# Kernel tuning notes

Hardware: AMD Instinct MI355X
Metric: run time of the kernel (lower is better)

## Reference

```python
import jax, jax.numpy as jnp
import numpy as np

EPS = 0.1
P, C, T_MLP, C_MLP, B = 196, 768, 384, 3072, 64


def yat(x, W, b, alpha):
    # x: (..., in), W: (out, in), b: (out,), alpha: (1,)
    dot_nb = jnp.einsum('...i,oi->...o', x, W)          # no-bias dot (shared GEMM)
    dot = dot_nb + b
    w_norm_sq = jnp.sum(W * W, axis=1)                   # (out,)
    x_norm_sq = jnp.sum(x * x, axis=-1, keepdims=True)   # (..., 1)
    dist_sq = w_norm_sq + x_norm_sq - 2.0 * dot_nb
    out_f = W.shape[0]
    scale_base = out_f / np.log(out_f + 1.0)
    scale = jnp.sqrt(jnp.asarray(scale_base, x.dtype)) ** alpha[0]
    return scale * (dot * dot) / (dist_sq + EPS)


def setup_inputs() -> dict:
    key = jax.random.key(0)
    ks = jax.random.split(key, 7)
    x = jax.random.normal(ks[0], (B, P, C), dtype=jnp.float32)
    # token-mixing YAT: in=P, out=T_MLP
    tw = jax.random.normal(ks[1], (T_MLP, P), dtype=jnp.float32) / np.sqrt(P)
    tb = jnp.zeros((T_MLP,), jnp.float32)
    t_alpha = jnp.ones((1,), jnp.float32)
    # token-mixing linear: T_MLP -> P
    w2 = jax.random.uniform(ks[2], (P, T_MLP), jnp.float32, -1, 1) / np.sqrt(T_MLP)
    b2 = jax.random.uniform(ks[3], (P,), jnp.float32, -1, 1) / np.sqrt(T_MLP)
    # channel-mixing YAT: in=C, out=C_MLP
    cw = jax.random.normal(ks[4], (C_MLP, C), dtype=jnp.float32) / np.sqrt(C)
    cb = jnp.zeros((C_MLP,), jnp.float32)
    c_alpha = jnp.ones((1,), jnp.float32)
    # channel-mixing linear: C_MLP -> C
    w4 = jax.random.uniform(ks[5], (C, C_MLP), jnp.float32, -1, 1) / np.sqrt(C_MLP)
    b4 = jax.random.uniform(ks[6], (C,), jnp.float32, -1, 1) / np.sqrt(C_MLP)
    return {"x": x, "tw": tw, "tb": tb, "t_alpha": t_alpha, "w2": w2, "b2": b2,
            "cw": cw, "cb": cb, "c_alpha": c_alpha, "w4": w4, "b4": b4}


def reference(x, tw, tb, t_alpha, w2, b2, cw, cb, c_alpha, w4, b4):
    # Token mixing (operates over patch dim)
    shortcut = x
    xt = jnp.swapaxes(x, 1, 2)                 # (B, C, P)
    h = yat(xt, tw, tb, t_alpha)               # (B, C, T_MLP)
    h = jnp.einsum('bct,pt->bcp', h, w2) + b2  # (B, C, P)
    x = shortcut + jnp.swapaxes(h, 1, 2)
    # Channel mixing (operates over hidden dim)
    shortcut = x
    h = yat(x, cw, cb, c_alpha)                # (B, P, C_MLP)
    h = jnp.einsum('bpm,cm->bpc', h, w4) + b4  # (B, P, C)
    return shortcut + h
```

## Files before the change

### kernel.cpp

```cpp
#include <hip/hip_runtime.h>
#include <hip/hip_bf16.h>
#include <math.h>

#define B_   64
#define P_   196
#define PPAD 224
#define C_   768
#define TM_  384
#define CM_  3072
#define EPSY 0.1f

typedef unsigned short u16;
typedef __attribute__((ext_vector_type(8))) short bf16x8;
typedef __attribute__((ext_vector_type(4))) float f32x4;

__device__ __forceinline__ float bf2f(u16 v) {
    return __uint_as_float(((unsigned int)v) << 16);
}
__device__ __forceinline__ u16 f2bf(float f) {
    unsigned int u = __float_as_uint(f);
    unsigned int rounding = 0x7FFFu + ((u >> 16) & 1u);
    return (u16)((u + rounding) >> 16);
}

__device__ __forceinline__ void gl_lds16(const u16* g, u16* l) {
    __builtin_amdgcn_global_load_lds(
        (const __attribute__((address_space(1))) unsigned int*)g,
        (__attribute__((address_space(3))) unsigned int*)l,
        16, 0, 0);
}


__global__ __launch_bounds__(256) void k_prep_xT(const float* __restrict__ x,
                                                 u16* __restrict__ xT,
                                                 float* __restrict__ xn1) {
    __shared__ u16 tile[32][33];
    __shared__ float colsum[32];
    const int b = blockIdx.z, p0 = blockIdx.x * 32, c0 = blockIdx.y * 32;
    const int tx = threadIdx.x & 31, ty = threadIdx.x >> 5;
    if (threadIdx.x < 32) colsum[threadIdx.x] = 0.f;
    const float* xb = x + (size_t)b * P_ * C_;
    float s = 0.f;
    #pragma unroll
    for (int r = 0; r < 4; ++r) {
        int p = p0 + ty + r * 8;
        float v = (p < P_) ? xb[(size_t)p * C_ + c0 + tx] : 0.f;
        u16 h = f2bf(v);
        tile[ty + r * 8][tx] = h;
        float vb = bf2f(h);
        s = fmaf(vb, vb, s);
    }
    __syncthreads();
    u16* dst = xT + ((size_t)b * C_ + c0) * PPAD + p0;
    #pragma unroll
    for (int r = 0; r < 4; ++r) {
        int cl = ty + r * 8;
        dst[(size_t)cl * PPAD + tx] = tile[tx][cl];
    }
    atomicAdd(&colsum[tx], s);
    __syncthreads();
    if (threadIdx.x < 32)
        atomicAdd(&xn1[(size_t)b * C_ + c0 + threadIdx.x], colsum[threadIdx.x]);
}

__device__ __forceinline__ void pad_norm_body(const float* in, u16* outb, float* norm,
                                              int rows, int inlen, int outlen,
                                              int bid, int tid) {
    int wave = (bid * 256 + tid) >> 6;
    int lane = tid & 63;
    if (wave >= rows) return;
    const float* src = in + (size_t)wave * inlen;
    u16* dst = outb + (size_t)wave * outlen;
    float s = 0.f;
    for (int i = lane; i < outlen; i += 64) {
        float v = (i < inlen) ? src[i] : 0.f;
        u16 h = f2bf(v);
        dst[i] = h;
        float vv = bf2f(h);
        s = fmaf(vv, vv, s);
    }
    #pragma unroll
    for (int off = 32; off > 0; off >>= 1) s += __shfl_down(s, off, 64);
    if (lane == 0) norm[wave] = s;
}

__global__ __launch_bounds__(256) void k_prep_weights(
    const float* __restrict__ tw, u16* __restrict__ twb, float* __restrict__ twn,
    const float* __restrict__ cw, u16* __restrict__ cwb, float* __restrict__ cwn,
    const float* __restrict__ w2, u16* __restrict__ w2b,
    const float* __restrict__ w4, u16* __restrict__ w4b) {
    int bid = blockIdx.x, tid = threadIdx.x;
    if (bid < 96) {
        pad_norm_body(tw, twb, twn, TM_, P_, PPAD, bid, tid);
    } else if (bid < 864) {
        pad_norm_body(cw, cwb, cwn, CM_, C_, C_, bid - 96, tid);
    } else if (bid < 1248) {
        int idx = (bid - 864) * 256 + tid;
        int row = idx / TM_;
        w2b[idx] = (row < P_) ? f2bf(w2[(size_t)row * TM_ + (idx % TM_)]) : (u16)0;
    } else {
        int idx = (bid - 1248) * 256 + tid;
        float4 v = ((const float4*)w4)[idx];
        ushort4 o;
        o.x = f2bf(v.x); o.y = f2bf(v.y); o.z = f2bf(v.z); o.w = f2bf(v.w);
        ((ushort4*)w4b)[idx] = o;
    }
}

__device__ __forceinline__ void mfma_mainloop(
    const u16* __restrict__ A, const u16* __restrict__ B,
    int lda, int ldb, int kiters,
    f32x4 (&acc)[4][4], u16* As, u16* Bs) {
    const int t = threadIdx.x;
    const int w = t >> 6, l = t & 63;
    const int quad = l >> 4, l15 = l & 15;
    const int row0 = t >> 2, kc = (t & 3) * 8;

    const u16* pa0 = A + (size_t)row0 * lda + kc;
    const u16* pa1 = A + (size_t)(64 + row0) * lda + kc;
    const u16* pb0 = B + (size_t)row0 * ldb + kc;
    const u16* pb1 = B + (size_t)(64 + row0) * ldb + kc;

    u16* ldsA0 = As + w * 512;
    u16* ldsA1 = As + 2048 + w * 512;
    u16* ldsB0 = Bs + w * 512;
    u16* ldsB1 = Bs + 2048 + w * 512;

#define STAGE_(bsel, koff)                          \
    do {                                            \
        const int nb_ = (bsel) * 4096;              \
        gl_lds16(pa0 + (koff), ldsA0 + nb_);        \
        gl_lds16(pa1 + (koff), ldsA1 + nb_);        \
        gl_lds16(pb0 + (koff), ldsB0 + nb_);        \
        gl_lds16(pb1 + (koff), ldsB1 + nb_);        \
    } while (0)

    STAGE_(0, 0);
    if (kiters > 1) {
        STAGE_(1, 32);
        asm volatile("s_waitcnt vmcnt(4)" ::: "memory");
    } else {
        asm volatile("s_waitcnt vmcnt(0)" ::: "memory");
    }
    __builtin_amdgcn_s_barrier();

    int cur = 0;
    int koff = 64;
    for (int it = 0; it < kiters; ++it) {
        const u16* Aw = As + cur * 4096 + (w >> 1) * 2048;
        const u16* Bw = Bs + cur * 4096 + (w & 1) * 2048;
        bf16x8 af[4], bfr[4];
        #pragma unroll
        for (int i = 0; i < 4; ++i)
            af[i] = *(const bf16x8*)(Aw + ((i * 16 + l15) * 32 + quad * 8));
        #pragma unroll
        for (int j = 0; j < 4; ++j)
            bfr[j] = *(const bf16x8*)(Bw + ((j * 16 + l15) * 32 + quad * 8));
        asm volatile("s_waitcnt lgkmcnt(0)" ::: "memory");
        __builtin_amdgcn_sched_barrier(0);
        __builtin_amdgcn_s_barrier();
        const bool more2 = (it + 2 < kiters);
        if (more2) { STAGE_(cur, koff); koff += 32; }
        __builtin_amdgcn_s_setprio(1);
        #pragma unroll
        for (int i = 0; i < 4; ++i)
            #pragma unroll
            for (int j = 0; j < 4; ++j)
                acc[i][j] = __builtin_amdgcn_mfma_f32_16x16x32_bf16(af[i], bfr[j], acc[i][j], 0, 0, 0);
        __builtin_amdgcn_s_setprio(0);
        if (it + 1 < kiters) {
            if (more2) asm volatile("s_waitcnt vmcnt(4)" ::: "memory");
            else       asm volatile("s_waitcnt vmcnt(0)" ::: "memory");
            __builtin_amdgcn_s_barrier();
        }
        cur ^= 1;
    }
#undef STAGE_
}

#define MFMA_CORE(AP, BP, LDA, LDB, KITERS)                              \
    __shared__ u16 As[2 * 128 * 32];                                     \
    __shared__ u16 Bs[2 * 128 * 32];                                     \
    const int t = threadIdx.x;                                           \
    const int wid = t >> 6, lane = t & 63;                               \
    const int quad = lane >> 4, l15 = lane & 15;                         \
    f32x4 acc[4][4];                                                     \
    _Pragma("unroll")                                                    \
    for (int i = 0; i < 4; ++i)                                          \
        _Pragma("unroll")                                                \
        for (int j = 0; j < 4; ++j) acc[i][j] = (f32x4){0.f,0.f,0.f,0.f};\
    mfma_mainloop(AP, BP, LDA, LDB, KITERS, acc, As, Bs);                \
    const int rbase = m0 + (wid >> 1) * 64;                              \
    const int cbase = n0 + (wid & 1) * 64;

#define PH_MID()  do { __builtin_amdgcn_sched_barrier(0);                 \
    __builtin_amdgcn_s_barrier();                                         \
    asm volatile("s_waitcnt lgkmcnt(0)" ::: "memory");                    \
    __builtin_amdgcn_sched_barrier(0);                                    \
    __builtin_amdgcn_s_setprio(1); } while (0)
#define PH_END()  do { __builtin_amdgcn_s_setprio(0);                     \
    __builtin_amdgcn_sched_barrier(0);                                    \
    __builtin_amdgcn_s_barrier(); } while (0)
#define PH_END_VM(n) do { __builtin_amdgcn_s_setprio(0);                  \
    asm volatile("s_waitcnt vmcnt(" #n ")" ::: "memory");                 \
    __builtin_amdgcn_sched_barrier(0);                                    \
    __builtin_amdgcn_s_barrier(); } while (0)

#define STG16(isB, d, h, T)                                               \
    gl_lds16(((isB) ? gB : gA) + (size_t)((h) * 128 + srow) *             \
                 ((isB) ? ldb : lda) + (T) * 64 + scol,                   \
             smem + ((isB) ? 32768 : 0) + (d) * 16384 + (h) * 8192 + t * 8)

#define DSA16(d, mh, Ar)                                                  \
    _Pragma("unroll")                                                     \
    for (int mi = 0; mi < 2; ++mi) {                                      \
        Ar[mi][0] = *(const bf16x8*)(aB0 + (d) * 16384 + ((mh) * 2 + mi) * 1024); \
        Ar[mi][1] = *(const bf16x8*)(aB1 + (d) * 16384 + ((mh) * 2 + mi) * 1024); \
    }
#define DSB16(d, nh, Br)                                                  \
    _Pragma("unroll")                                                     \
    for (int ni = 0; ni < 2; ++ni) {                                      \
        Br[ni][0] = *(const bf16x8*)(bB0 + (d) * 16384 + ((nh) * 2 + ni) * 1024); \
        Br[ni][1] = *(const bf16x8*)(bB1 + (d) * 16384 + ((nh) * 2 + ni) * 1024); \
    }
#define MMQ16(mh, nh, Br)                                                 \
    _Pragma("unroll")                                                     \
    for (int kk = 0; kk < 2; ++kk)                                        \
        _Pragma("unroll")                                                 \
        for (int mi = 0; mi < 2; ++mi)                                    \
            _Pragma("unroll")                                             \
            for (int ni = 0; ni < 2; ++ni)                                \
                acc[(mh) * 2 + mi][(nh) * 2 + ni] =                       \
                    __builtin_amdgcn_mfma_f32_16x16x32_bf16(              \
                        a[mi][kk], Br[ni][kk],                            \
                        acc[(mh) * 2 + mi][(nh) * 2 + ni], 0, 0, 0);

__device__ __forceinline__ void mfma16w_mainloop(
    const u16* __restrict__ A, const u16* __restrict__ B,
    int lda, int ldb, int ntiles,
    f32x4 (&acc)[4][4], u16* smem) {
    const int t = threadIdx.x;
    const int w = t >> 6, lane = t & 63;
    const int wr = w >> 2, wc = w & 3;
    const int quad = lane >> 4, l15 = lane & 15;

    const int srow = t >> 3;
    const int scol = (((t & 7) ^ (srow & 7)) << 3);
    const u16* gA = A;
    const u16* gB = B;

    const int q = (quad * 8) ^ ((l15 & 7) << 3);
    const u16* aB0 = smem + (wr * 64 + l15) * 64 + q;
    const u16* aB1 = smem + (wr * 64 + l15) * 64 + (q ^ 32);
    const u16* bB0 = smem + 32768 + (wc * 64 + l15) * 64 + q;
    const u16* bB1 = smem + 32768 + (wc * 64 + l15) * 64 + (q ^ 32);

    STG16(1, 0, 0, 0); STG16(1, 0, 1, 0);
    STG16(0, 0, 0, 0); STG16(0, 0, 1, 0);
    STG16(1, 1, 0, 1); STG16(1, 1, 1, 1);
    asm volatile("s_waitcnt vmcnt(2)" ::: "memory");
    __builtin_amdgcn_s_barrier();

    bf16x8 a[2][2], b[2][2], c[2][2];
    const int NI = ntiles >> 1;
    for (int i = 0; i < NI - 1; ++i) {
        const int T1 = 2 * i + 1, N0 = 2 * i + 2, N1 = 2 * i + 3;
        DSA16(0, 0, a) DSB16(0, 0, b)
        STG16(0, 1, 0, T1);
        PH_MID(); MMQ16(0, 0, b) PH_END();
        DSB16(0, 1, c)
        STG16(0, 1, 1, T1);
        PH_MID(); MMQ16(0, 1, c) PH_END();
        DSA16(0, 1, a)
        STG16(1, 0, 0, N0);
        PH_MID(); MMQ16(1, 1, c) PH_END();
        STG16(1, 0, 1, N0);
        PH_MID(); MMQ16(1, 0, b) PH_END_VM(2);
        DSA16(1, 0, a) DSB16(1, 0, b)
        STG16(0, 0, 0, N0);
        PH_MID(); MMQ16(0, 0, b) PH_END();
        DSB16(1, 1, c)
        STG16(0, 0, 1, N0);
        PH_MID(); MMQ16(0, 1, c) PH_END();
        DSA16(1, 1, a)
        STG16(1, 1, 0, N1);
        PH_MID(); MMQ16(1, 1, c) PH_END();
        STG16(1, 1, 1, N1);
        PH_MID(); MMQ16(1, 0, b) PH_END_VM(2);
    }
    {
        const int T1 = ntiles - 1;
        DSA16(0, 0, a) DSB16(0, 0, b)
        STG16(0, 1, 0, T1);
        PH_MID(); MMQ16(0, 0, b) PH_END();
        DSB16(0, 1, c)
        STG16(0, 1, 1, T1);
        PH_MID(); MMQ16(0, 1, c) PH_END();
        DSA16(0, 1, a)
        PH_MID(); MMQ16(1, 1, c) PH_END();
        PH_MID(); MMQ16(1, 0, b) PH_END_VM(0);
        DSA16(1, 0, a) DSB16(1, 0, b)
        PH_MID(); MMQ16(0, 0, b) PH_END();
        DSB16(1, 1, c)
        PH_MID(); MMQ16(0, 1, c) PH_END();
        DSA16(1, 1, a)
        PH_MID(); MMQ16(1, 1, c) PH_END();
        PH_MID(); MMQ16(1, 0, b)
        __builtin_amdgcn_s_setprio(0);
    }
}

__global__ __launch_bounds__(256) void k1_token_yat(
    const u16* __restrict__ xT, const u16* __restrict__ twb,
    const float* __restrict__ tb, const float* __restrict__ twn,
    const float* __restrict__ xn1, const float* __restrict__ alpha, float sb,
    u16* __restrict__ h1) {
    const int m0 = (blockIdx.x + blockIdx.y * 8) * 128;
    const int n0 = blockIdx.z * 128;
    MFMA_CORE(xT + (size_t)m0 * PPAD, twb + (size_t)n0 * PPAD, PPAD, PPAD, PPAD / 32)
    float scale = powf(sqrtf(sb), alpha[0]);
    #pragma unroll
    for (int i = 0; i < 4; ++i) {
        #pragma unroll
        for (int j = 0; j < 4; ++j) {
            int col = cbase + j * 16 + l15;
            float bn = tb[col], wnn = twn[col];
            #pragma unroll
            for (int reg = 0; reg < 4; ++reg) {
                int row = rbase + i * 16 + quad * 4 + reg;
                float dnb = acc[i][j][reg];
                float dot = dnb + bn;
                float dist = wnn + xn1[row] - 2.f * dnb;
                h1[(size_t)row * TM_ + col] = f2bf(scale * dot * dot / (dist + EPSY));
            }
        }
    }
}

__global__ __launch_bounds__(1024) void k3_chan_yat(
    const u16* __restrict__ x1b, const u16* __restrict__ cwb,
    const float* __restrict__ cb, const float* __restrict__ cwn,
    const float* __restrict__ xn2, const float* __restrict__ alpha, float sb,
    u16* __restrict__ h3) {
    __shared__ __align__(16) u16 smem[65536];
    const int mt = blockIdx.x + blockIdx.y * 8;
    if (mt >= (B_ * P_) / 256) return;
    const int m0 = mt * 256;
    const int n0 = blockIdx.z * 256;
    const int t = threadIdx.x;
    const int w = t >> 6, l = t & 63;
    const int wr = w >> 2, wc = w & 3;
    const int quad = l >> 4, l15 = l & 15;
    f32x4 acc[4][4];
    #pragma unroll
    for (int m = 0; m < 4; ++m)
        #pragma unroll
        for (int n = 0; n < 4; ++n) acc[m][n] = (f32x4){0.f, 0.f, 0.f, 0.f};
    mfma16w_mainloop(x1b + (size_t)m0 * C_, cwb + (size_t)n0 * C_,
                     C_, C_, C_ / 64, acc, smem);
    const int rbase = m0 + wr * 64;
    const int cbase = n0 + wc * 64;
    float scale = powf(sqrtf(sb), alpha[0]);
    #pragma unroll
    for (int m = 0; m < 4; ++m) {
        #pragma unroll
        for (int n = 0; n < 4; ++n) {
            int col = cbase + n * 16 + l15;
            float bn = cb[col], wnn = cwn[col];
            #pragma unroll
            for (int reg = 0; reg < 4; ++reg) {
                int row = rbase + m * 16 + quad * 4 + reg;
                float dnb = acc[m][n][reg];
                float dot = dnb + bn;
                float dist = wnn + xn2[row] - 2.f * dnb;
                h3[(size_t)row * CM_ + col] = f2bf(scale * dot * dot / (dist + EPSY));
            }
        }
    }
}

__global__ __launch_bounds__(256) void k2_token_out(
    const u16* __restrict__ w2b, const u16* __restrict__ h1,
    const float* __restrict__ b2, const float* __restrict__ x,
    float* __restrict__ xn2, u16* __restrict__ x1b) {
    const int m0 = blockIdx.x * 128, n0 = blockIdx.y * 128;
    const u16* Bz = h1 + (size_t)blockIdx.z * C_ * TM_;
    MFMA_CORE(w2b + (size_t)m0 * TM_, Bz + (size_t)n0 * TM_, TM_, TM_, TM_ / 32)
    const float* rz = x + (size_t)blockIdx.z * P_ * C_;
    u16* oz = x1b + (size_t)blockIdx.z * P_ * C_;
    float* xrow = xn2 + (size_t)blockIdx.z * P_;
    #pragma unroll
    for (int i = 0; i < 4; ++i) {
        #pragma unroll
        for (int reg = 0; reg < 4; ++reg) {
            int row = rbase + i * 16 + quad * 4 + reg;
            if (row < P_) {
                float bm = b2[row];
                float s = 0.f;
                #pragma unroll
                for (int j = 0; j < 4; ++j) {
                    int col = cbase + j * 16 + l15;
                    float v = acc[i][j][reg] + bm + rz[(size_t)row * C_ + col];
                    u16 h = f2bf(v);
                    oz[(size_t)row * C_ + col] = h;
                    float vb = bf2f(h);
                    s = fmaf(vb, vb, s);
                }
                s += __shfl_xor(s, 1, 64);
                s += __shfl_xor(s, 2, 64);
                s += __shfl_xor(s, 4, 64);
                s += __shfl_xor(s, 8, 64);
                if (l15 == 0) atomicAdd(&xrow[row], s);
            }
        }
    }
}

__global__ __launch_bounds__(1024) void k4_split(
    const u16* __restrict__ h3, const u16* __restrict__ w4b,
    u16* __restrict__ pbuf, int KK) {
    __shared__ __align__(16) u16 smem[65536];
    const int mt = blockIdx.x + blockIdx.y * 8;
    if (mt >= (B_ * P_) / 256) return;
    const int m0 = mt * 256;
    const int nz = blockIdx.z;
    const int n0 = (nz % 3) * 256;
    const int ks = nz / 3;
    const int kbase = ks * KK;
    const int t = threadIdx.x;
    const int w = t >> 6, l = t & 63;
    const int wr = w >> 2, wc = w & 3;
    const int quad = l >> 4, l15 = l & 15;
    f32x4 acc[4][4];
    #pragma unroll
    for (int m = 0; m < 4; ++m)
        #pragma unroll
        for (int n = 0; n < 4; ++n) acc[m][n] = (f32x4){0.f, 0.f, 0.f, 0.f};
    mfma16w_mainloop(h3 + (size_t)m0 * CM_ + kbase, w4b + (size_t)n0 * CM_ + kbase,
                     CM_, CM_, KK / 64, acc, smem);
    const int rbase = m0 + wr * 64;
    const int cbase = n0 + wc * 64;
    u16* dst = pbuf + (size_t)ks * ((size_t)B_ * P_ * C_);
    #pragma unroll
    for (int m = 0; m < 4; ++m) {
        #pragma unroll
        for (int n = 0; n < 4; ++n) {
            int col = cbase + n * 16 + l15;
            #pragma unroll
            for (int reg = 0; reg < 4; ++reg) {
                int row = rbase + m * 16 + quad * 4 + reg;
                dst[(size_t)row * C_ + col] = f2bf(acc[m][n][reg]);
            }
        }
    }
}

template <int NS>
__global__ __launch_bounds__(256) void k4_reduce(
    float* __restrict__ outp, const u16* __restrict__ pbuf,
    const u16* __restrict__ x1b, const float* __restrict__ b4) {
    int idx = blockIdx.x * 256 + threadIdx.x;
    int c = (idx * 4) % C_;
    ushort4 r = ((const ushort4*)x1b)[idx];
    float4 o;
    o.x = bf2f(r.x) + b4[c + 0];
    o.y = bf2f(r.y) + b4[c + 1];
    o.z = bf2f(r.z) + b4[c + 2];
    o.w = bf2f(r.w) + b4[c + 3];
    const size_t stride4 = (size_t)B_ * P_ * C_ / 4;
    #pragma unroll
    for (int s = 0; s < NS; ++s) {
        ushort4 p = ((const ushort4*)pbuf)[idx + s * stride4];
        o.x += bf2f(p.x); o.y += bf2f(p.y); o.z += bf2f(p.z); o.w += bf2f(p.w);
    }
    ((float4*)outp)[idx] = o;
}

__global__ __launch_bounds__(256) void gemm_k4_fb(
    const u16* __restrict__ A, const u16* __restrict__ Bmat,
    const float* __restrict__ biasN, const u16* __restrict__ resB,
    float* __restrict__ Fout) {
    __shared__ u16 As[128 * 32];
    __shared__ u16 Bs[64 * 32];
    const int t = threadIdx.x;
    const int wid = t >> 6, lane = t & 63;
    const int quad = lane >> 4, l15 = lane & 15;
    const int m0 = blockIdx.x * 128, n0 = blockIdx.y * 64;
    f32x4 acc[4][2];
    #pragma unroll
    for (int i = 0; i < 4; ++i)
        #pragma unroll
        for (int j = 0; j < 2; ++j) acc[i][j] = (f32x4){0.f, 0.f, 0.f, 0.f};
    const u16* Aw = As + (wid >> 1) * (64 * 32);
    const u16* Bw = Bs + (wid & 1) * (32 * 32);
    const int arow = t >> 2, akc = (t & 3) * 8;
    for (int k0 = 0; k0 < CM_; k0 += 32) {
        gl_lds16(A + (size_t)(m0 + arow) * CM_ + k0 + akc,      As + wid * 512);
        gl_lds16(A + (size_t)(m0 + 64 + arow) * CM_ + k0 + akc, As + 2048 + wid * 512);
        gl_lds16(Bmat + (size_t)(n0 + arow) * CM_ + k0 + akc,   Bs + wid * 512);
        __syncthreads();
        bf16x8 af[4], bfr[2];
        #pragma unroll
        for (int i = 0; i < 4; ++i)
            af[i] = *(const bf16x8*)(Aw + ((i * 16 + l15) * 32 + quad * 8));
        #pragma unroll
        for (int j = 0; j < 2; ++j)
            bfr[j] = *(const bf16x8*)(Bw + ((j * 16 + l15) * 32 + quad * 8));
        #pragma unroll
        for (int i = 0; i < 4; ++i)
            #pragma unroll
            for (int j = 0; j < 2; ++j)
                acc[i][j] = __builtin_amdgcn_mfma_f32_16x16x32_bf16(af[i], bfr[j], acc[i][j], 0, 0, 0);
        __syncthreads();
    }
    const int rbase = m0 + (wid >> 1) * 64;
    const int cbase = n0 + (wid & 1) * 32;
    #pragma unroll
    for (int i = 0; i < 4; ++i) {
        #pragma unroll
        for (int j = 0; j < 2; ++j) {
            int col = cbase + j * 16 + l15;
            float bn = biasN[col];
            #pragma unroll
            for (int reg = 0; reg < 4; ++reg) {
                int row = rbase + i * 16 + quad * 4 + reg;
                float v = acc[i][j][reg] + bn + bf2f(resB[(size_t)row * C_ + col]);
                Fout[(size_t)row * C_ + col] = v;
            }
        }
    }
}

extern "C" void kernel_launch(void* const* d_in, const int* in_sizes, int n_in,
                              void* d_out, int out_size, void* d_ws, size_t ws_size,
                              hipStream_t stream) {
    const float* x  = (const float*)d_in[0];
    const float* tw = (const float*)d_in[1];
    const float* tb = (const float*)d_in[2];
    const float* ta = (const float*)d_in[3];
    const float* w2 = (const float*)d_in[4];
    const float* b2 = (const float*)d_in[5];
    const float* cw = (const float*)d_in[6];
    const float* cb = (const float*)d_in[7];
    const float* ca = (const float*)d_in[8];
    const float* w4 = (const float*)d_in[9];
    const float* b4 = (const float*)d_in[10];
    float* out = (float*)d_out;

    char* ws = (char*)d_ws;
    u16* h1 = (u16*)ws;
    u16* xT = (u16*)(ws + 37748736);
    u16* h3 = (u16*)ws;
    size_t off = 77070336;
    u16* x1b = (u16*)(ws + off); off += (size_t)B_ * P_ * C_ * 2;
    u16* twb = (u16*)(ws + off); off += (size_t)TM_ * PPAD * 2;
    u16* w2b = (u16*)(ws + off); off += (size_t)256 * TM_ * 2;
    u16* cwb = (u16*)(ws + off); off += (size_t)CM_ * C_ * 2;
    u16* w4b = (u16*)(ws + off); off += (size_t)C_ * CM_ * 2;
    float* xn1 = (float*)(ws + off); off += (size_t)B_ * C_ * 4;
    float* xn2 = (float*)(ws + off); off += (size_t)B_ * P_ * 4;
    float* twn = (float*)(ws + off); off += (size_t)TM_ * 4;
    float* cwn = (float*)(ws + off); off += (size_t)CM_ * 4;
    u16* pbuf = (u16*)(ws + off);
    const size_t psz = (size_t)B_ * P_ * C_ * 2;

    int nsplit = 1;
    if (ws_size >= off + 4 * psz)      nsplit = 4;
    else if (ws_size >= off + 2 * psz) nsplit = 2;

    const float SBT = (float)TM_ / logf((float)TM_ + 1.0f);
    const float SBC = (float)CM_ / logf((float)CM_ + 1.0f);

    hipMemsetAsync(xn1, 0, (size_t)(B_ * C_ + B_ * P_) * 4, stream);
    k_prep_weights<<<3552, 256, 0, stream>>>(tw, twb, twn, cw, cwb, cwn,
                                             w2, w2b, w4, w4b);
    k_prep_xT<<<dim3(PPAD / 32, C_ / 32, B_), 256, 0, stream>>>(x, xT, xn1);

    k1_token_yat<<<dim3(8, 48, 3), 256, 0, stream>>>(
        xT, twb, tb, twn, xn1, ta, SBT, h1);

    k2_token_out<<<dim3(2, C_ / 128, B_), 256, 0, stream>>>(
        w2b, h1, b2, x, xn2, x1b);

    k3_chan_yat<<<dim3(8, 7, 12), 1024, 0, stream>>>(
        x1b, cwb, cb, cwn, xn2, ca, SBC, h3);

    if (nsplit > 1) {
        k4_split<<<dim3(8, 7, 3 * nsplit), 1024, 0, stream>>>(
            h3, w4b, pbuf, CM_ / nsplit);
        int n4 = B_ * P_ * C_ / 4;
        if (nsplit == 4)
            k4_reduce<4><<<(n4 + 255) / 256, 256, 0, stream>>>(out, pbuf, x1b, b4);
        else
            k4_reduce<2><<<(n4 + 255) / 256, 256, 0, stream>>>(out, pbuf, x1b, b4);
    } else {
        gemm_k4_fb<<<dim3(B_ * P_ / 128, C_ / 64), 256, 0, stream>>>(
            h3, w4b, b4, x1b, out);
    }
}
```

Baseline: 438.8 us.

## Shrink channel-mixing GEMM tiles from 256x256/1024 threads to 128x128/256 threads

Replaces the 256x256 tile, 16-wave main loop used by the channel YAT and split-K output GEMMs with a 128x128 tile, 4-wave variant that uses half the LDS. Each thread now issues two global-to-LDS loads per stage, so the vmcnt waits are adjusted to match. The grids are enlarged so there are more, smaller blocks, which should fill the CUs better and allow several blocks per CU. The trade-off is less operand reuse per tile and more global and L2 traffic.

```diff
diff --git a/kernel.cpp b/kernel.cpp
--- a/kernel.cpp
+++ b/kernel.cpp
@@ -206,24 +206,29 @@
     __builtin_amdgcn_sched_barrier(0);                                    \
     __builtin_amdgcn_s_barrier(); } while (0)
 
-#define STG16(isB, d, h, T)                                               \
-    gl_lds16(((isB) ? gB : gA) + (size_t)((h) * 128 + srow) *             \
-                 ((isB) ? ldb : lda) + (T) * 64 + scol,                   \
-             smem + ((isB) ? 32768 : 0) + (d) * 16384 + (h) * 8192 + t * 8)
-
-#define DSA16(d, mh, Ar)                                                  \
+#define STG4(isB, d, h, T)                                                \
+    do {                                                                  \
+        const int ld_ = (isB) ? ldb : lda;                                \
+        const u16* g_ = ((isB) ? gB : gA) +                               \
+            (size_t)((h) * 64 + srow) * ld_ + (T) * 64 + scol;            \
+        u16* s_ = smem + ((isB) ? 16384 : 0) + (d) * 8192 + (h) * 4096 + t * 8; \
+        gl_lds16(g_, s_);                                                 \
+        gl_lds16(g_ + (size_t)32 * ld_, s_ + 2048);                       \
+    } while (0)
+
+#define DSA4(d, mh, Ar)                                                   \
     _Pragma("unroll")                                                     \
     for (int mi = 0; mi < 2; ++mi) {                                      \
-        Ar[mi][0] = *(const bf16x8*)(aB0 + (d) * 16384 + ((mh) * 2 + mi) * 1024); \
-        Ar[mi][1] = *(const bf16x8*)(aB1 + (d) * 16384 + ((mh) * 2 + mi) * 1024); \
-    }
-#define DSB16(d, nh, Br)                                                  \
+        Ar[mi][0] = *(const bf16x8*)(aB0 + (d) * 8192 + ((mh) * 2 + mi) * 1024); \
+        Ar[mi][1] = *(const bf16x8*)(aB1 + (d) * 8192 + ((mh) * 2 + mi) * 1024); \
+    }
+#define DSB4(d, nh, Br)                                                   \
     _Pragma("unroll")                                                     \
     for (int ni = 0; ni < 2; ++ni) {                                      \
-        Br[ni][0] = *(const bf16x8*)(bB0 + (d) * 16384 + ((nh) * 2 + ni) * 1024); \
-        Br[ni][1] = *(const bf16x8*)(bB1 + (d) * 16384 + ((nh) * 2 + ni) * 1024); \
-    }
-#define MMQ16(mh, nh, Br)                                                 \
+        Br[ni][0] = *(const bf16x8*)(bB0 + (d) * 8192 + ((nh) * 2 + ni) * 1024); \
+        Br[ni][1] = *(const bf16x8*)(bB1 + (d) * 8192 + ((nh) * 2 + ni) * 1024); \
+    }
+#define MMQ4(mh, nh, Br)                                                  \
     _Pragma("unroll")                                                     \
     for (int kk = 0; kk < 2; ++kk)                                        \
         _Pragma("unroll")                                                 \
@@ -235,77 +240,75 @@
                         a[mi][kk], Br[ni][kk],                            \
                         acc[(mh) * 2 + mi][(nh) * 2 + ni], 0, 0, 0);
 
-__device__ __forceinline__ void mfma16w_mainloop(
-    const u16* __restrict__ A, const u16* __restrict__ B,
+__device__ __forceinline__ void mfma128_8p(
+    const u16* __restrict__ gA, const u16* __restrict__ gB,
     int lda, int ldb, int ntiles,
     f32x4 (&acc)[4][4], u16* smem) {
     const int t = threadIdx.x;
     const int w = t >> 6, lane = t & 63;
-    const int wr = w >> 2, wc = w & 3;
+    const int wr = w >> 1, wc = w & 1;
     const int quad = lane >> 4, l15 = lane & 15;
 
     const int srow = t >> 3;
     const int scol = (((t & 7) ^ (srow & 7)) << 3);
-    const u16* gA = A;
-    const u16* gB = B;
 
     const int q = (quad * 8) ^ ((l15 & 7) << 3);
     const u16* aB0 = smem + (wr * 64 + l15) * 64 + q;
     const u16* aB1 = smem + (wr * 64 + l15) * 64 + (q ^ 32);
-    const u16* bB0 = smem + 32768 + (wc * 64 + l15) * 64 + q;
-    const u16* bB1 = smem + 32768 + (wc * 64 + l15) * 64 + (q ^ 32);
-
-    STG16(1, 0, 0, 0); STG16(1, 0, 1, 0);
-    STG16(0, 0, 0, 0); STG16(0, 0, 1, 0);
-    STG16(1, 1, 0, 1); STG16(1, 1, 1, 1);
-    asm volatile("s_waitcnt vmcnt(2)" ::: "memory");
+    const u16* bB0 = smem + 16384 + (wc * 64 + l15) * 64 + q;
+    const u16* bB1 = smem + 16384 + (wc * 64 + l15) * 64 + (q ^ 32);
+
+    STG4(0, 0, 0, 0); STG4(0, 0, 1, 0);
+    STG4(1, 0, 0, 0); STG4(1, 0, 1, 0);
+    STG4(1, 1, 0, 1); STG4(1, 1, 1, 1);
+    asm volatile("s_waitcnt vmcnt(4)" ::: "memory");
     __builtin_amdgcn_s_barrier();
 
     bf16x8 a[2][2], b[2][2], c[2][2];
     const int NI = ntiles >> 1;
     for (int i = 0; i < NI - 1; ++i) {
         const int T1 = 2 * i + 1, N0 = 2 * i + 2, N1 = 2 * i + 3;
-        DSA16(0, 0, a) DSB16(0, 0, b)
-        STG16(0, 1, 0, T1);
-        PH_MID(); MMQ16(0, 0, b) PH_END();
-        DSB16(0, 1, c)
-        STG16(0, 1, 1, T1);
-        PH_MID(); MMQ16(0, 1, c) PH_END();
-        DSA16(0, 1, a)
-        STG16(1, 0, 0, N0);
-        PH_MID(); MMQ16(1, 1, c) PH_END();
-        STG16(1, 0, 1, N0);
-        PH_MID(); MMQ16(1, 0, b) PH_END_VM(2);
-        DSA16(1, 0, a) DSB16(1, 0, b)
-        STG16(0, 0, 0, N0);
-        PH_MID(); MMQ16(0, 0, b) PH_END();
-        DSB16(1, 1, c)
-        STG16(0, 0, 1, N0);
-        PH_MID(); MMQ16(0, 1, c) PH_END();
-        DSA16(1, 1, a)
-        STG16(1, 1, 0, N1);
-        PH_MID(); MMQ16(1, 1, c) PH_END();
-        STG16(1, 1, 1, N1);
-        PH_MID(); MMQ16(1, 0, b) PH_END_VM(2);
+        DSA4(0, 0, a) DSB4(0, 0, b)
+        STG4(0, 1, 0, T1);
+        PH_MID(); MMQ4(0, 0, b) PH_END();
+        DSB4(0, 1, c)
+        STG4(0, 1, 1, T1);
+        PH_MID(); MMQ4(0, 1, c) PH_END();
+        DSA4(0, 1, a)
+        STG4(1, 0, 0, N0);
+        PH_MID(); MMQ4(1, 1, c) PH_END();
+        STG4(1, 0, 1, N0);
+        PH_MID(); MMQ4(1, 0, b) PH_END_VM(4);
+        DSA4(1, 0, a) DSB4(1, 0, b)
+        STG4(0, 0, 0, N0);
+        PH_MID(); MMQ4(0, 0, b) PH_END();
+        DSB4(1, 1, c)
+        STG4(0, 0, 1, N0);
+        PH_MID(); MMQ4(0, 1, c) PH_END();
+        DSA4(1, 1, a)
+        STG4(1, 1, 0, N1);
+        PH_MID(); MMQ4(1, 1, c) PH_END();
+        STG4(1, 1, 1, N1);
+        PH_MID(); MMQ4(1, 0, b) PH_END_VM(4);
     }
     {
-        const int T1 = ntiles - 1;
-        DSA16(0, 0, a) DSB16(0, 0, b)
-        STG16(0, 1, 0, T1);
-        PH_MID(); MMQ16(0, 0, b) PH_END();
-        DSB16(0, 1, c)
-        STG16(0, 1, 1, T1);
-        PH_MID(); MMQ16(0, 1, c) PH_END();
-        DSA16(0, 1, a)
-        PH_MID(); MMQ16(1, 1, c) PH_END();
-        PH_MID(); MMQ16(1, 0, b) PH_END_VM(0);
-        DSA16(1, 0, a) DSB16(1, 0, b)
-        PH_MID(); MMQ16(0, 0, b) PH_END();
-        DSB16(1, 1, c)
-        PH_MID(); MMQ16(0, 1, c) PH_END();
-        DSA16(1, 1, a)
-        PH_MID(); MMQ16(1, 1, c) PH_END();
-        PH_MID(); MMQ16(1, 0, b)
+        const int Tl = ntiles - 1;
+        DSA4(0, 0, a) DSB4(0, 0, b)
+        STG4(0, 1, 0, Tl);
+        PH_MID(); MMQ4(0, 0, b) PH_END();
+        DSB4(0, 1, c)
+        STG4(0, 1, 1, Tl);
+        PH_MID(); MMQ4(0, 1, c) PH_END();
+        DSA4(0, 1, a)
+        PH_MID(); MMQ4(1, 1, c) PH_END();
+        PH_MID(); MMQ4(1, 0, b) PH_END_VM(0);
+        DSA4(1, 0, a) DSB4(1, 0, b)
+        PH_MID(); MMQ4(0, 0, b) PH_END();
+        DSB4(1, 1, c)
+        PH_MID(); MMQ4(0, 1, c) PH_END();
+        DSA4(1, 1, a)
+        PH_MID(); MMQ4(1, 1, c) PH_END();
+        PH_MID(); MMQ4(1, 0, b)
         __builtin_amdgcn_s_setprio(0);
     }
 }
@@ -337,27 +340,27 @@
     }
 }
 
-__global__ __launch_bounds__(1024) void k3_chan_yat(
+__global__ __launch_bounds__(256) void k3_chan_yat(
     const u16* __restrict__ x1b, const u16* __restrict__ cwb,
     const float* __restrict__ cb, const float* __restrict__ cwn,
     const float* __restrict__ xn2, const float* __restrict__ alpha, float sb,
     u16* __restrict__ h3) {
-    __shared__ __align__(16) u16 smem[65536];
+    __shared__ __align__(16) u16 smem[32768];
     const int mt = blockIdx.x + blockIdx.y * 8;
-    if (mt >= (B_ * P_) / 256) return;
-    const int m0 = mt * 256;
-    const int n0 = blockIdx.z * 256;
+    if (mt >= (B_ * P_) / 128) return;
+    const int m0 = mt * 128;
+    const int n0 = blockIdx.z * 128;
     const int t = threadIdx.x;
     const int w = t >> 6, l = t & 63;
-    const int wr = w >> 2, wc = w & 3;
+    const int wr = w >> 1, wc = w & 1;
     const int quad = l >> 4, l15 = l & 15;
     f32x4 acc[4][4];
     #pragma unroll
     for (int m = 0; m < 4; ++m)
         #pragma unroll
         for (int n = 0; n < 4; ++n) acc[m][n] = (f32x4){0.f, 0.f, 0.f, 0.f};
-    mfma16w_mainloop(x1b + (size_t)m0 * C_, cwb + (size_t)n0 * C_,
-                     C_, C_, C_ / 64, acc, smem);
+    mfma128_8p(x1b + (size_t)m0 * C_, cwb + (size_t)n0 * C_,
+               C_, C_, C_ / 64, acc, smem);
     const int rbase = m0 + wr * 64;
     const int cbase = n0 + wc * 64;
     float scale = powf(sqrtf(sb), alpha[0]);
@@ -416,28 +419,28 @@
     }
 }
 
-__global__ __launch_bounds__(1024) void k4_split(
+__global__ __launch_bounds__(256) void k4_split(
     const u16* __restrict__ h3, const u16* __restrict__ w4b,
     u16* __restrict__ pbuf, int KK) {
-    __shared__ __align__(16) u16 smem[65536];
+    __shared__ __align__(16) u16 smem[32768];
     const int mt = blockIdx.x + blockIdx.y * 8;
-    if (mt >= (B_ * P_) / 256) return;
-    const int m0 = mt * 256;
+    if (mt >= (B_ * P_) / 128) return;
+    const int m0 = mt * 128;
     const int nz = blockIdx.z;
-    const int n0 = (nz % 3) * 256;
-    const int ks = nz / 3;
+    const int n0 = (nz % (C_ / 128)) * 128;
+    const int ks = nz / (C_ / 128);
     const int kbase = ks * KK;
     const int t = threadIdx.x;
     const int w = t >> 6, l = t & 63;
-    const int wr = w >> 2, wc = w & 3;
+    const int wr = w >> 1, wc = w & 1;
     const int quad = l >> 4, l15 = l & 15;
     f32x4 acc[4][4];
     #pragma unroll
     for (int m = 0; m < 4; ++m)
         #pragma unroll
         for (int n = 0; n < 4; ++n) acc[m][n] = (f32x4){0.f, 0.f, 0.f, 0.f};
-    mfma16w_mainloop(h3 + (size_t)m0 * CM_ + kbase, w4b + (size_t)n0 * CM_ + kbase,
-                     CM_, CM_, KK / 64, acc, smem);
+    mfma128_8p(h3 + (size_t)m0 * CM_ + kbase, w4b + (size_t)n0 * CM_ + kbase,
+               CM_, CM_, KK / 64, acc, smem);
     const int rbase = m0 + wr * 64;
     const int cbase = n0 + wc * 64;
     u16* dst = pbuf + (size_t)ks * ((size_t)B_ * P_ * C_);
@@ -582,11 +585,11 @@
     k2_token_out<<<dim3(2, C_ / 128, B_), 256, 0, stream>>>(
         w2b, h1, b2, x, xn2, x1b);
 
-    k3_chan_yat<<<dim3(8, 7, 12), 1024, 0, stream>>>(
+    k3_chan_yat<<<dim3(8, 13, 24), 256, 0, stream>>>(
         x1b, cwb, cb, cwn, xn2, ca, SBC, h3);
 
     if (nsplit > 1) {
-        k4_split<<<dim3(8, 7, 3 * nsplit), 1024, 0, stream>>>(
+        k4_split<<<dim3(8, 13, (C_ / 128) * nsplit), 256, 0, stream>>>(
             h3, w4b, pbuf, CM_ / nsplit);
         int n4 = B_ * P_ * C_ / 4;
         if (nsplit == 4)
```

Measured after the change: 365.2 us, median of 2. 16.8% less time.
